# Kernel optimization log

Hardware: AMD Instinct MI355X
Metric: run time of the kernel (lower is better)

## Reference

```python
import jax, jax.numpy as jnp
import numpy as np

H = 16          # num_heads
EPS = 1e-5      # torch LayerNorm default eps


def setup_inputs() -> dict:
    key = jax.random.key(0)
    ks = jax.random.split(key, 12)
    B, S, D = 4, 2048, 1024
    sc = 1.0 / np.sqrt(D)
    return {
        "queries": jax.random.normal(ks[0], (B, S, D), jnp.float32),
        "keys": jax.random.normal(ks[1], (B, S, D), jnp.float32),
        "values": jax.random.normal(ks[2], (B, S, D), jnp.float32),
        "attention_mask": jax.random.randint(ks[3], (B, S), 0, 2, jnp.int32),
        "Wq": jax.random.normal(ks[4], (D, D), jnp.float32) * sc,
        "bq": jnp.zeros((D,), jnp.float32),
        "Wk": jax.random.normal(ks[5], (D, D), jnp.float32) * sc,
        "bk": jnp.zeros((D,), jnp.float32),
        "Wv": jax.random.normal(ks[6], (D, D), jnp.float32) * sc,
        "bv": jnp.zeros((D,), jnp.float32),
        "gamma": jnp.ones((D,), jnp.float32),
        "beta": jnp.zeros((D,), jnp.float32),
    }


def reference(queries, keys, values, attention_mask, Wq, bq, Wk, bk, Wv, bv, gamma, beta):
    B, S, D = queries.shape
    dh = D // H

    # QKV projections with ReLU epilogue (nn.Sequential(Linear, ReLU))
    q = jax.nn.relu(jnp.einsum("bsd,de->bse", queries, Wq) + bq)
    k = jax.nn.relu(jnp.einsum("bsd,de->bse", keys, Wk) + bk)
    v = jax.nn.relu(jnp.einsum("bsd,de->bse", values, Wv) + bv)

    # chunk along last dim + stack at dim=1  ==  [B,S,H,dh] -> [B,H,S,dh]
    q_ = q.reshape(B, S, H, dh).transpose(0, 2, 1, 3)
    k_ = k.reshape(B, S, H, dh).transpose(0, 2, 1, 3)
    v_ = v.reshape(B, S, H, dh).transpose(0, 2, 1, 3)

    # scaled dot-product scores [B,H,S,S]
    scores = jnp.einsum("bhqd,bhkd->bhqk", q_, k_) / jnp.sqrt(jnp.float32(dh))

    # mask[b,h,i,j] = attention_mask[b,i]; masked positions set to 1e-9
    # (faithful to torch.masked_fill(value=1e-09) in the original)
    m = attention_mask[:, None, :, None].astype(bool)  # [B,1,S,1]
    scores = jnp.where(m, scores, jnp.float32(1e-9))

    a = jax.nn.softmax(scores, axis=-1)
    o = jnp.einsum("bhqk,bhkd->bhqd", a, v_)          # [B,H,S,dh]
    o = o.transpose(0, 2, 1, 3).reshape(B, S, D)

    # residual + LayerNorm
    x = o + queries
    mu = jnp.mean(x, axis=-1, keepdims=True)
    var = jnp.mean(jnp.square(x - mu), axis=-1, keepdims=True)
    return (x - mu) * jax.lax.rsqrt(var + EPS) * gamma + beta
```

## Files before the change

kernel.cpp:

```cpp
#include <hip/hip_runtime.h>
#include <hip/hip_bf16.h>
#include <stdint.h>

typedef __bf16 bf16x8 __attribute__((ext_vector_type(8)));
typedef float f32x4 __attribute__((ext_vector_type(4)));
typedef float f32x16 __attribute__((ext_vector_type(16)));
typedef unsigned short ushort8v __attribute__((ext_vector_type(8)));
typedef unsigned short ushort4v __attribute__((ext_vector_type(4)));
typedef uint32_t uint4v __attribute__((ext_vector_type(4)));

#define MFMA16(a, b, c) __builtin_amdgcn_mfma_f32_16x16x32_bf16(a, b, c, 0, 0, 0)
#define MFMA32(a, b, c) __builtin_amdgcn_mfma_f32_32x32x16_bf16(a, b, c, 0, 0, 0)

#define GLOAD_LDS16(g, l)                                                        \
    __builtin_amdgcn_global_load_lds(                                            \
        (const __attribute__((address_space(1))) uint32_t*)(g),                  \
        (__attribute__((address_space(3))) uint32_t*)(l), 16, 0, 0)

__device__ __forceinline__ unsigned short f2bf_u(float f) {
    union { float f; uint32_t u; } cv; cv.f = f;
    uint32_t u = cv.u;
    uint32_t r = (u + 0x7FFFu + ((u >> 16) & 1u)) >> 16;
    return (unsigned short)r;
}

__device__ __forceinline__ uint32_t pkbf(float a, float b) {
    union { __hip_bfloat162 h; uint32_t u; } cv;
    cv.h = __float22bfloat162_rn(make_float2(a, b));
    return cv.u;
}

__device__ __forceinline__ float fexp2(float x) { return __builtin_amdgcn_exp2f(x); }

__global__ __launch_bounds__(256) void wt_cast(const float* __restrict__ W0,
                                               const float* __restrict__ W1,
                                               const float* __restrict__ W2,
                                               unsigned short* __restrict__ T0,
                                               unsigned short* __restrict__ T1,
                                               unsigned short* __restrict__ T2) {
    const int z = blockIdx.z;
    const float* W = z == 0 ? W0 : (z == 1 ? W1 : W2);
    unsigned short* Wt = z == 0 ? T0 : (z == 1 ? T1 : T2);
    __shared__ float t[32][33];
    const int tx = threadIdx.x & 31, ty = threadIdx.x >> 5;
    const int n0 = blockIdx.x * 32, k0 = blockIdx.y * 32;
#pragma unroll
    for (int i = 0; i < 4; i++) {
        int r = i * 8 + ty;
        t[r][tx] = W[(size_t)(k0 + r) * 1024 + n0 + tx];
    }
    __syncthreads();
#pragma unroll
    for (int i = 0; i < 4; i++) {
        int r = i * 8 + ty;
        Wt[(size_t)(n0 + r) * 1024 + k0 + tx] = f2bf_u(t[tx][r]);
    }
}

__global__ __launch_bounds__(256) void acast(const float* __restrict__ A0,
                                             const float* __restrict__ A1,
                                             const float* __restrict__ A2,
                                             unsigned short* __restrict__ B0,
                                             unsigned short* __restrict__ B1,
                                             unsigned short* __restrict__ B2) {
    const int z = blockIdx.y;
    const float* A = z == 0 ? A0 : (z == 1 ? A1 : A2);
    unsigned short* B = z == 0 ? B0 : (z == 1 ? B1 : B2);
    const size_t i = ((size_t)blockIdx.x * 256 + threadIdx.x) * 8;
    const float4 f0 = *reinterpret_cast<const float4*>(A + i);
    const float4 f1 = *reinterpret_cast<const float4*>(A + i + 4);
    uint4v u;
    u[0] = pkbf(f0.x, f0.y);
    u[1] = pkbf(f0.z, f0.w);
    u[2] = pkbf(f1.x, f1.y);
    u[3] = pkbf(f1.z, f1.w);
    *reinterpret_cast<uint4v*>(B + i) = u;
}

__global__ __launch_bounds__(256) void qkv_gemm3(
    const unsigned short* __restrict__ Aq, const unsigned short* __restrict__ Ak,
    const unsigned short* __restrict__ Av,
    const unsigned short* __restrict__ Wq, const unsigned short* __restrict__ Wk,
    const unsigned short* __restrict__ Wv,
    const float* __restrict__ biasq, const float* __restrict__ biask,
    const float* __restrict__ biasv,
    unsigned short* __restrict__ outq, unsigned short* __restrict__ outk,
    unsigned short* __restrict__ outv) {
    __shared__ __align__(16) unsigned short aS[2][128 * 32];
    __shared__ __align__(16) unsigned short wS[2][128 * 32];
    const int id = blockIdx.x;
    const int xcd = id & 7;
    const int local = id >> 3;
    const int z = local >> 6;
    const int l2i = local & 63;
    const int m0 = (xcd * 8 + (l2i >> 3)) * 128;
    const int n0 = (l2i & 7) * 128;

    const unsigned short* A = z == 0 ? Aq : (z == 1 ? Ak : Av);
    const unsigned short* Wt = z == 0 ? Wq : (z == 1 ? Wk : Wv);
    const float* bias = z == 0 ? biasq : (z == 1 ? biask : biasv);
    unsigned short* out = z == 0 ? outq : (z == 1 ? outk : outv);
    const bool vt = (z == 2);

    const int tid = threadIdx.x;
    const int lane = tid & 63, wave = tid >> 6;
    const int rrow = lane & 15, rgrp = lane >> 4;
    const int wm = wave >> 1, wn = wave & 1;

    const int row0 = tid >> 2, c0 = tid & 3;
    const int row1 = (tid + 256) >> 2;
    const int arow_f = wm * 64 + rrow;
    const int brow_f = wn * 64 + rrow;

    f32x4 acc[4][4];
#pragma unroll
    for (int i = 0; i < 4; i++)
#pragma unroll
        for (int j = 0; j < 4; j++) acc[i][j] = (f32x4)0.0f;

    auto STAGE = [&](const unsigned short* src, int r0, int k0, void* dstbase) {
        char* dst = (char*)dstbase + wave * 1024;
        GLOAD_LDS16((const char*)src + ((size_t)(r0 + row0) * 1024 + k0 + c0 * 8) * 2, dst);
        GLOAD_LDS16((const char*)src + ((size_t)(r0 + row1) * 1024 + k0 + c0 * 8) * 2,
                    dst + 4096);
    };

    STAGE(A, m0, 0, &aS[0][0]);
    STAGE(Wt, n0, 0, &wS[0][0]);
    __syncthreads();

    for (int ks = 0; ks < 32; ks++) {
        const int cur = ks & 1;
        if (ks < 31) {
            STAGE(A, m0, (ks + 1) * 32, &aS[cur ^ 1][0]);
            STAGE(Wt, n0, (ks + 1) * 32, &wS[cur ^ 1][0]);
        }

        bf16x8 af[4], bfr[4];
#pragma unroll
        for (int mi = 0; mi < 4; mi++)
            af[mi] = *reinterpret_cast<const bf16x8*>(
                (const char*)&aS[cur][0] + (arow_f + mi * 16) * 64 + rgrp * 16);
#pragma unroll
        for (int ni = 0; ni < 4; ni++)
            bfr[ni] = *reinterpret_cast<const bf16x8*>(
                (const char*)&wS[cur][0] + (brow_f + ni * 16) * 64 + rgrp * 16);
        __builtin_amdgcn_s_setprio(1);
#pragma unroll
        for (int mi = 0; mi < 4; mi++)
#pragma unroll
            for (int ni = 0; ni < 4; ni++)
                acc[mi][ni] = MFMA16(af[mi], bfr[ni], acc[mi][ni]);
        __builtin_amdgcn_s_setprio(0);

        __syncthreads();
    }

#pragma unroll
    for (int mi = 0; mi < 4; mi++) {
#pragma unroll
        for (int ni = 0; ni < 4; ni++) {
            const int n = n0 + wn * 64 + ni * 16 + rrow;
            const float bv = bias[n];
            const int h = n >> 6, d = n & 63;
            const int mbase = m0 + wm * 64 + mi * 16 + rgrp * 4;
            const int b = mbase >> 11, s = mbase & 2047;
            if (vt) {
                ushort4v pv;
#pragma unroll
                for (int jr = 0; jr < 4; jr++)
                    pv[jr] = f2bf_u(fmaxf(acc[mi][ni][jr] + bv, 0.0f));
                *reinterpret_cast<ushort4v*>(out + ((size_t)((b * 16 + h) * 64 + d)) * 2048 + s) = pv;
            } else {
#pragma unroll
                for (int jr = 0; jr < 4; jr++)
                    out[((size_t)((b * 16 + h) * 2048 + (s + jr))) * 64 + d] =
                        f2bf_u(fmaxf(acc[mi][ni][jr] + bv, 0.0f));
            }
        }
    }
}

__global__ __launch_bounds__(256, 4) void flash_attn(const unsigned short* __restrict__ Qg,
                                                     const unsigned short* __restrict__ Kg,
                                                     const unsigned short* __restrict__ Vt,
                                                     const int* __restrict__ mask,
                                                     float* __restrict__ O) {
    __shared__ __align__(16) unsigned short ldsK[2][64 * 64];
    __shared__ __align__(16) unsigned short ldsV[2][64 * 64];
    const int tid = threadIdx.x;
    const int lane = tid & 63, wave = tid >> 6;
    const int c = lane & 31, hi = lane >> 5;
    const int bid = blockIdx.x;
    const int swzb = (bid & 7) * 128 + (bid >> 3);
    const int gid = swzb * 4 + wave;
    const int bh = gid >> 6;
    const int q0 = (gid & 63) * 32;
    const int b = bh >> 4, h = bh & 15;
    const size_t base = (size_t)bh * (2048 * 64);
    const unsigned short* Qb = Qg + base;
    const unsigned short* Kb = Kg + base;
    const unsigned short* Vb = Vt + base;

    const int srow = lane >> 3;
    const int schunk = (lane & 7) ^ srow;
    int offL[4], offH[4];
#pragma unroll
    for (int ds = 0; ds < 4; ds++) {
        offL[ds] = c * 128 + ((((ds << 1) + hi) ^ (c & 7)) << 4);
        offH[ds] = offL[ds] + 32 * 128;
    }

    bf16x8 qf[4];
#pragma unroll
    for (int ds = 0; ds < 4; ds++)
        qf[ds] = *reinterpret_cast<const bf16x8*>(Qb + (size_t)(q0 + c) * 64 + ds * 16 + hi * 8);

    const int mk = mask[b * 2048 + q0 + c];
    const float sc = mk ? 0.1803368801f : 0.0f;

    union { uint32_t u[4]; bf16x8 v; } onesf;
#pragma unroll
    for (int i = 0; i < 4; i++) onesf.u[i] = 0x3F803F80u;

    f32x16 lacc = (f32x16)0.0f;
    f32x16 oacc0 = (f32x16)0.0f, oacc1 = (f32x16)0.0f;

    auto STAGE = [&](int kt, int bufi) {
        const char* ktile = (const char*)Kb + (size_t)kt * 8192;
        const char* vtile = (const char*)Vb + (size_t)kt * 128;
        char* kdst = (char*)&ldsK[bufi][0] + wave * 2048;
        char* vdst = (char*)&ldsV[bufi][0] + wave * 2048;
#pragma unroll
        for (int i = 0; i < 2; i++) {
            const int row = wave * 16 + i * 8 + srow;
            GLOAD_LDS16(ktile + row * 128 + schunk * 16, kdst + i * 1024);
            GLOAD_LDS16(vtile + (size_t)row * 4096 + schunk * 16, vdst + i * 1024);
        }
    };

    STAGE(0, 0);
    __syncthreads();

    for (int kt = 0; kt < 32; kt++) {
        const int cur = kt & 1;
        if (kt < 31) STAGE(kt + 1, cur ^ 1);
        const char* kbuf = (const char*)&ldsK[cur][0];
        const char* vbuf = (const char*)&ldsV[cur][0];

        f32x16 sacc0 = (f32x16)0.0f, sacc1 = (f32x16)0.0f;
        __builtin_amdgcn_s_setprio(1);
#pragma unroll
        for (int ds = 0; ds < 4; ds++) {
            bf16x8 k0 = *reinterpret_cast<const bf16x8*>(kbuf + offL[ds]);
            bf16x8 k1 = *reinterpret_cast<const bf16x8*>(kbuf + offH[ds]);
            sacc0 = MFMA32(k0, qf[ds], sacc0);
            sacc1 = MFMA32(k1, qf[ds], sacc1);
        }
        __builtin_amdgcn_s_setprio(0);

#pragma unroll
        for (int j = 0; j < 16; j++) {
            sacc0[j] = fexp2(sacc0[j] * sc);
            sacc1[j] = fexp2(sacc1[j] * sc);
        }

        {
            uint32_t w0[8];
#pragma unroll
            for (int i = 0; i < 8; i++) w0[i] = pkbf(sacc0[2 * i], sacc0[2 * i + 1]);
            uint32_t s00 = __shfl_xor(hi ? w0[0] : w0[2], 32, 64);
            uint32_t s01 = __shfl_xor(hi ? w0[1] : w0[3], 32, 64);
            uint32_t s02 = __shfl_xor(hi ? w0[4] : w0[6], 32, 64);
            uint32_t s03 = __shfl_xor(hi ? w0[5] : w0[7], 32, 64);
            union { uint32_t u[4]; bf16x8 v; } pa[2];
            if (hi == 0) {
                pa[0].u[0] = w0[0]; pa[0].u[1] = w0[1]; pa[0].u[2] = s00; pa[0].u[3] = s01;
                pa[1].u[0] = w0[4]; pa[1].u[1] = w0[5]; pa[1].u[2] = s02; pa[1].u[3] = s03;
            } else {
                pa[0].u[0] = s00; pa[0].u[1] = s01; pa[0].u[2] = w0[2]; pa[0].u[3] = w0[3];
                pa[1].u[0] = s02; pa[1].u[1] = s03; pa[1].u[2] = w0[6]; pa[1].u[3] = w0[7];
            }
            __builtin_amdgcn_s_setprio(1);
#pragma unroll
            for (int ks = 0; ks < 2; ks++) {
                bf16x8 v0 = *reinterpret_cast<const bf16x8*>(vbuf + offL[ks]);
                bf16x8 v1 = *reinterpret_cast<const bf16x8*>(vbuf + offH[ks]);
                lacc = MFMA32(pa[ks].v, onesf.v, lacc);
                oacc0 = MFMA32(pa[ks].v, v0, oacc0);
                oacc1 = MFMA32(pa[ks].v, v1, oacc1);
            }
            __builtin_amdgcn_s_setprio(0);
        }
        {
            uint32_t w1[8];
#pragma unroll
            for (int i = 0; i < 8; i++) w1[i] = pkbf(sacc1[2 * i], sacc1[2 * i + 1]);
            uint32_t s10 = __shfl_xor(hi ? w1[0] : w1[2], 32, 64);
            uint32_t s11 = __shfl_xor(hi ? w1[1] : w1[3], 32, 64);
            uint32_t s12 = __shfl_xor(hi ? w1[4] : w1[6], 32, 64);
            uint32_t s13 = __shfl_xor(hi ? w1[5] : w1[7], 32, 64);
            union { uint32_t u[4]; bf16x8 v; } pa[2];
            if (hi == 0) {
                pa[0].u[0] = w1[0]; pa[0].u[1] = w1[1]; pa[0].u[2] = s10; pa[0].u[3] = s11;
                pa[1].u[0] = w1[4]; pa[1].u[1] = w1[5]; pa[1].u[2] = s12; pa[1].u[3] = s13;
            } else {
                pa[0].u[0] = s10; pa[0].u[1] = s11; pa[0].u[2] = w1[2]; pa[0].u[3] = w1[3];
                pa[1].u[0] = s12; pa[1].u[1] = s13; pa[1].u[2] = w1[6]; pa[1].u[3] = w1[7];
            }
            __builtin_amdgcn_s_setprio(1);
#pragma unroll
            for (int ks = 0; ks < 2; ks++) {
                bf16x8 v0 = *reinterpret_cast<const bf16x8*>(vbuf + offL[2 + ks]);
                bf16x8 v1 = *reinterpret_cast<const bf16x8*>(vbuf + offH[2 + ks]);
                lacc = MFMA32(pa[ks].v, onesf.v, lacc);
                oacc0 = MFMA32(pa[ks].v, v0, oacc0);
                oacc1 = MFMA32(pa[ks].v, v1, oacc1);
            }
            __builtin_amdgcn_s_setprio(0);
        }

        __syncthreads();
    }

#pragma unroll
    for (int reg = 0; reg < 16; reg++) {
        const int rr = (reg & 3) + 8 * (reg >> 2) + 4 * hi;
        const float ir = 1.0f / lacc[reg];
        const size_t rowoff = (size_t)(b * 2048 + q0 + rr) * 1024 + h * 64 + c;
        O[rowoff]      = oacc0[reg] * ir;
        O[rowoff + 32] = oacc1[reg] * ir;
    }
}

__global__ __launch_bounds__(256) void resid_ln(const float* __restrict__ O,
                                                const float* __restrict__ Qin,
                                                const float* __restrict__ gamma,
                                                const float* __restrict__ beta,
                                                float* __restrict__ out) {
    __shared__ float red[4];
    const int row = blockIdx.x, tid = threadIdx.x;
    const size_t base = (size_t)row * 1024 + tid * 4;
    float4 o4 = *reinterpret_cast<const float4*>(O + base);
    float4 q4 = *reinterpret_cast<const float4*>(Qin + base);
    float x0 = o4.x + q4.x, x1 = o4.y + q4.y, x2 = o4.z + q4.z, x3 = o4.w + q4.w;

    float s = x0 + x1 + x2 + x3;
#pragma unroll
    for (int off = 32; off >= 1; off >>= 1) s += __shfl_xor(s, off, 64);
    const int w = tid >> 6;
    if ((tid & 63) == 0) red[w] = s;
    __syncthreads();
    const float mean = (red[0] + red[1] + red[2] + red[3]) * (1.0f / 1024.0f);
    __syncthreads();

    const float d0 = x0 - mean, d1 = x1 - mean, d2 = x2 - mean, d3 = x3 - mean;
    float vs = d0 * d0 + d1 * d1 + d2 * d2 + d3 * d3;
#pragma unroll
    for (int off = 32; off >= 1; off >>= 1) vs += __shfl_xor(vs, off, 64);
    if ((tid & 63) == 0) red[w] = vs;
    __syncthreads();
    const float var = (red[0] + red[1] + red[2] + red[3]) * (1.0f / 1024.0f);
    const float rstd = rsqrtf(var + 1e-5f);

    float4 g = *reinterpret_cast<const float4*>(gamma + tid * 4);
    float4 be = *reinterpret_cast<const float4*>(beta + tid * 4);
    float4 r;
    r.x = d0 * rstd * g.x + be.x;
    r.y = d1 * rstd * g.y + be.y;
    r.z = d2 * rstd * g.z + be.z;
    r.w = d3 * rstd * g.w + be.w;
    *reinterpret_cast<float4*>(out + base) = r;
}

extern "C" void kernel_launch(void* const* d_in, const int* in_sizes, int n_in,
                              void* d_out, int out_size, void* d_ws, size_t ws_size,
                              hipStream_t stream) {
    const float* q_in = (const float*)d_in[0];
    const float* k_in = (const float*)d_in[1];
    const float* v_in = (const float*)d_in[2];
    const int* mask = (const int*)d_in[3];
    const float* Wq = (const float*)d_in[4];
    const float* bq = (const float*)d_in[5];
    const float* Wk = (const float*)d_in[6];
    const float* bk = (const float*)d_in[7];
    const float* Wv = (const float*)d_in[8];
    const float* bv = (const float*)d_in[9];
    const float* gamma = (const float*)d_in[10];
    const float* beta = (const float*)d_in[11];
    float* out = (float*)d_out;

    unsigned short* wtq = (unsigned short*)d_ws;
    unsigned short* wtk = wtq + 1024 * 1024;
    unsigned short* wtv = wtk + 1024 * 1024;
    unsigned short* Qb = wtv + 1024 * 1024;
    unsigned short* Kb = Qb + 8192 * 1024;
    unsigned short* Vtb = Kb + 8192 * 1024;
    unsigned short* Aqb = Vtb + 8192 * 1024;
    unsigned short* Akb = Aqb + 8192 * 1024;
    unsigned short* Avb = Akb + 8192 * 1024;
    float* Obuf = (float*)Aqb;

    dim3 tb(256);
    wt_cast<<<dim3(32, 32, 3), tb, 0, stream>>>(Wq, Wk, Wv, wtq, wtk, wtv);
    acast<<<dim3(4096, 3), tb, 0, stream>>>(q_in, k_in, v_in, Aqb, Akb, Avb);
    qkv_gemm3<<<dim3(1536), tb, 0, stream>>>(Aqb, Akb, Avb, wtq, wtk, wtv,
                                             bq, bk, bv, Qb, Kb, Vtb);
    flash_attn<<<dim3(1024), tb, 0, stream>>>(Qb, Kb, Vtb, mask, Obuf);
    resid_ln<<<dim3(8192), tb, 0, stream>>>(Obuf, q_in, gamma, beta, out);
}
```

Before: 206.9 us.

## Fold mask and softmax scale into Q epilogue, store attention output as bf16

The QKV GEMM epilogue now multiplies Q by the log2e/sqrt(dh) scale, or by zero for masked rows. This removes the per-element multiply before exp2 in the flash-attention inner loop. The attention output buffer changes from fp32 to bf16, which halves its write traffic and the read traffic in the residual LayerNorm kernel. In exchange, Q is rounded to bf16 after scaling and the attention output loses precision before the residual add.

```diff
diff --git a/kernel.cpp b/kernel.cpp
--- a/kernel.cpp
+++ b/kernel.cpp
@@ -17,11 +17,19 @@
         (const __attribute__((address_space(1))) uint32_t*)(g),                  \
         (__attribute__((address_space(3))) uint32_t*)(l), 16, 0, 0)
 
+#define QSCALE 0.1803368801f
+
 __device__ __forceinline__ unsigned short f2bf_u(float f) {
     union { float f; uint32_t u; } cv; cv.f = f;
     uint32_t u = cv.u;
     uint32_t r = (u + 0x7FFFu + ((u >> 16) & 1u)) >> 16;
     return (unsigned short)r;
+}
+
+__device__ __forceinline__ float bf2f(unsigned short u) {
+    union { uint32_t u; float f; } cv;
+    cv.u = (uint32_t)u << 16;
+    return cv.f;
 }
 
 __device__ __forceinline__ uint32_t pkbf(float a, float b) {
@@ -83,7 +91,7 @@
     const unsigned short* __restrict__ Wq, const unsigned short* __restrict__ Wk,
     const unsigned short* __restrict__ Wv,
     const float* __restrict__ biasq, const float* __restrict__ biask,
-    const float* __restrict__ biasv,
+    const float* __restrict__ biasv, const int* __restrict__ mask,
     unsigned short* __restrict__ outq, unsigned short* __restrict__ outk,
     unsigned short* __restrict__ outv) {
     __shared__ __align__(16) unsigned short aS[2][128 * 32];
@@ -158,13 +166,17 @@
 
 #pragma unroll
     for (int mi = 0; mi < 4; mi++) {
+        const int mbase = m0 + wm * 64 + mi * 16 + rgrp * 4;
+        const int b = mbase >> 11, s = mbase & 2047;
+        float qs[4];
+#pragma unroll
+        for (int jr = 0; jr < 4; jr++)
+            qs[jr] = (z != 0) ? 1.0f : (mask[b * 2048 + s + jr] ? QSCALE : 0.0f);
 #pragma unroll
         for (int ni = 0; ni < 4; ni++) {
             const int n = n0 + wn * 64 + ni * 16 + rrow;
             const float bv = bias[n];
             const int h = n >> 6, d = n & 63;
-            const int mbase = m0 + wm * 64 + mi * 16 + rgrp * 4;
-            const int b = mbase >> 11, s = mbase & 2047;
             if (vt) {
                 ushort4v pv;
 #pragma unroll
@@ -175,7 +187,7 @@
 #pragma unroll
                 for (int jr = 0; jr < 4; jr++)
                     out[((size_t)((b * 16 + h) * 2048 + (s + jr))) * 64 + d] =
-                        f2bf_u(fmaxf(acc[mi][ni][jr] + bv, 0.0f));
+                        f2bf_u(fmaxf(acc[mi][ni][jr] + bv, 0.0f) * qs[jr]);
             }
         }
     }
@@ -184,8 +196,7 @@
 __global__ __launch_bounds__(256, 4) void flash_attn(const unsigned short* __restrict__ Qg,
                                                      const unsigned short* __restrict__ Kg,
                                                      const unsigned short* __restrict__ Vt,
-                                                     const int* __restrict__ mask,
-                                                     float* __restrict__ O) {
+                                                     unsigned short* __restrict__ O) {
     __shared__ __align__(16) unsigned short ldsK[2][64 * 64];
     __shared__ __align__(16) unsigned short ldsV[2][64 * 64];
     const int tid = threadIdx.x;
@@ -216,9 +227,6 @@
     for (int ds = 0; ds < 4; ds++)
         qf[ds] = *reinterpret_cast<const bf16x8*>(Qb + (size_t)(q0 + c) * 64 + ds * 16 + hi * 8);
 
-    const int mk = mask[b * 2048 + q0 + c];
-    const float sc = mk ? 0.1803368801f : 0.0f;
-
     union { uint32_t u[4]; bf16x8 v; } onesf;
 #pragma unroll
     for (int i = 0; i < 4; i++) onesf.u[i] = 0x3F803F80u;
@@ -261,8 +269,8 @@
 
 #pragma unroll
         for (int j = 0; j < 16; j++) {
-            sacc0[j] = fexp2(sacc0[j] * sc);
-            sacc1[j] = fexp2(sacc1[j] * sc);
+            sacc0[j] = fexp2(sacc0[j]);
+            sacc1[j] = fexp2(sacc1[j]);
         }
 
         {
@@ -328,12 +336,12 @@
         const int rr = (reg & 3) + 8 * (reg >> 2) + 4 * hi;
         const float ir = 1.0f / lacc[reg];
         const size_t rowoff = (size_t)(b * 2048 + q0 + rr) * 1024 + h * 64 + c;
-        O[rowoff]      = oacc0[reg] * ir;
-        O[rowoff + 32] = oacc1[reg] * ir;
-    }
-}
-
-__global__ __launch_bounds__(256) void resid_ln(const float* __restrict__ O,
+        O[rowoff]      = f2bf_u(oacc0[reg] * ir);
+        O[rowoff + 32] = f2bf_u(oacc1[reg] * ir);
+    }
+}
+
+__global__ __launch_bounds__(256) void resid_ln(const unsigned short* __restrict__ O,
                                                 const float* __restrict__ Qin,
                                                 const float* __restrict__ gamma,
                                                 const float* __restrict__ beta,
@@ -341,9 +349,10 @@
     __shared__ float red[4];
     const int row = blockIdx.x, tid = threadIdx.x;
     const size_t base = (size_t)row * 1024 + tid * 4;
-    float4 o4 = *reinterpret_cast<const float4*>(O + base);
-    float4 q4 = *reinterpret_cast<const float4*>(Qin + base);
-    float x0 = o4.x + q4.x, x1 = o4.y + q4.y, x2 = o4.z + q4.z, x3 = o4.w + q4.w;
+    const ushort4v o4 = *reinterpret_cast<const ushort4v*>(O + base);
+    const float4 q4 = *reinterpret_cast<const float4*>(Qin + base);
+    float x0 = bf2f(o4[0]) + q4.x, x1 = bf2f(o4[1]) + q4.y;
+    float x2 = bf2f(o4[2]) + q4.z, x3 = bf2f(o4[3]) + q4.w;
 
     float s = x0 + x1 + x2 + x3;
 #pragma unroll
@@ -399,13 +408,13 @@
     unsigned short* Aqb = Vtb + 8192 * 1024;
     unsigned short* Akb = Aqb + 8192 * 1024;
     unsigned short* Avb = Akb + 8192 * 1024;
-    float* Obuf = (float*)Aqb;
+    unsigned short* Obuf = Aqb;
 
     dim3 tb(256);
     wt_cast<<<dim3(32, 32, 3), tb, 0, stream>>>(Wq, Wk, Wv, wtq, wtk, wtv);
     acast<<<dim3(4096, 3), tb, 0, stream>>>(q_in, k_in, v_in, Aqb, Akb, Avb);
     qkv_gemm3<<<dim3(1536), tb, 0, stream>>>(Aqb, Akb, Avb, wtq, wtk, wtv,
-                                             bq, bk, bv, Qb, Kb, Vtb);
-    flash_attn<<<dim3(1024), tb, 0, stream>>>(Qb, Kb, Vtb, mask, Obuf);
+                                             bq, bk, bv, mask, Qb, Kb, Vtb);
+    flash_attn<<<dim3(1024), tb, 0, stream>>>(Qb, Kb, Vtb, Obuf);
     resid_ln<<<dim3(8192), tb, 0, stream>>>(Obuf, q_in, gamma, beta, out);
 }
```

Result: faster. 197.9 us (-4.4%).
